# Performance work log

Measured on AMD Instinct MI355X. Metric: run time of the kernel, lower is better.

The kernel has to match this reference:

```python
import jax, jax.numpy as jnp
from jax import lax
import numpy as np
import math

B = 8
DIFF_LEN, HORIZON, NUM_NODES = 336, 96, 1024
SEG_LEN, D_CONV, D_MODEL = 8, 64, 128
NUM_KERNELS, DEPTH, ALPHA = 6, 2, 0.05
FREQ = math.ceil(DIFF_LEN / SEG_LEN)      # 42
STEP = math.ceil(HORIZON / SEG_LEN)       # 12
PAD = SEG_LEN * FREQ - DIFF_LEN           # 0 here, code stays general
MAXK = 2 * NUM_KERNELS - 1                # 11


def setup_inputs() -> dict:
    key = jax.random.key(0)
    ks = iter(jax.random.split(key, 64))
    p = lambda *s: 0.02 * jax.random.normal(next(ks), s, jnp.float32)
    inp = dict(
        x_diff=jax.random.normal(next(ks), (B, DIFF_LEN, NUM_NODES), jnp.float32),
        adj=jax.random.uniform(next(ks), (NUM_NODES, NUM_NODES), jnp.float32),
        enc_w1=p(SEG_LEN, D_MODEL), enc_b1=p(D_MODEL),
        enc_w2=p(D_MODEL, D_CONV), enc_b2=p(D_CONV),
        dec_w1=p(D_CONV, D_MODEL), dec_b1=p(D_MODEL),
        dec_w2=p(D_MODEL, SEG_LEN), dec_b2=p(SEG_LEN),
        g1_w=p((DEPTH + 1) * D_CONV, D_CONV), g1_b=p(D_CONV),
        g2_w=p((DEPTH + 1) * D_CONV, D_CONV), g2_b=p(D_CONV),
    )
    for i in range(NUM_KERNELS):
        inp[f'conv_w{i}'] = p(D_CONV, D_CONV, 1, 2 * i + 1)
        inp[f'conv_b{i}'] = p(D_CONV)
    return inp


def _mlp(x, w1, b1, w2, b2):
    # 2-hidden-layer MLP with ReLU (dropout = identity at eval)
    return jnp.maximum(x @ w1 + b1, 0.0) @ w2 + b2


def _t_inception(x, conv_ws, conv_bs):
    # x: (B, D, N, T); inception = mean of 'same'-padded (1, 2i+1) convs
    out = jnp.zeros_like(x)
    for i, (w, b) in enumerate(zip(conv_ws, conv_bs)):
        out = out + lax.conv_general_dilated(
            x, w, (1, 1), ((0, 0), (i, i)),
            dimension_numbers=('NCHW', 'OIHW', 'NCHW')) + b[None, :, None, None]
    return out / len(conv_ws)


def _norm_adj(adj):
    a = adj + jnp.eye(adj.shape[0], dtype=adj.dtype)
    return a / a.sum(1, keepdims=True)


def _mixprop(x, a, w, b):
    # x: (B, T, N, D), a: row-normalized (N, N)
    h = x
    outs = [h]
    for _ in range(DEPTH):
        h = ALPHA * x + (1.0 - ALPHA) * jnp.einsum('vn,btnd->btvd', a, h)
        outs.append(h)
    return jnp.concatenate(outs, -1) @ w + b


def _stconv(x, a1, a2, conv_ws, conv_bs, g1_w, g1_b, g2_w, g2_b):
    res = jnp.transpose(x, (0, 3, 2, 1))            # b d n t
    res = _t_inception(res, conv_ws, conv_bs)
    res = jnp.transpose(res, (0, 3, 2, 1))          # b t n d
    res = _mixprop(res, a1, g1_w, g1_b) + _mixprop(res, a2, g2_w, g2_b)
    return res + x                                   # dropout = identity at eval


def reference(x_diff, adj,
              enc_w1, enc_b1, enc_w2, enc_b2,
              dec_w1, dec_b1, dec_w2, dec_b2,
              g1_w, g1_b, g2_w, g2_b,
              conv_w0, conv_b0, conv_w1, conv_b1, conv_w2, conv_b2,
              conv_w3, conv_b3, conv_w4, conv_b4, conv_w5, conv_b5):
    conv_ws = [conv_w0, conv_w1, conv_w2, conv_w3, conv_w4, conv_w5]
    conv_bs = [conv_b0, conv_b1, conv_b2, conv_b3, conv_b4, conv_b5]
    Bb, L, N = x_diff.shape
    a1 = _norm_adj(adj)
    a2 = _norm_adj(adj.T)

    # segment + left-pad with tail so length = FREQ * SEG_LEN
    res = jnp.concatenate((x_diff[:, L - PAD:, :], x_diff), axis=1)
    res = res.reshape(Bb, FREQ, SEG_LEN, N)
    res = jnp.transpose(res, (0, 1, 3, 2))          # (B, F, N, P)
    res = _mlp(res, enc_w1, enc_b1, enc_w2, enc_b2)  # (B, F, N, D)

    # reconstruction branch (teacher-forced one-step shift)
    rec = jnp.concatenate(
        (res[:, :1],
         _stconv(res[:, :-1], a1, a2, conv_ws, conv_bs, g1_w, g1_b, g2_w, g2_b)),
        axis=1)
    rec = _mlp(rec, dec_w1, dec_b1, dec_w2, dec_b2)  # (B, F, N, P)
    rec = jnp.transpose(rec, (0, 1, 3, 2)).reshape(Bb, FREQ * SEG_LEN, N)
    rec = rec[:, -DIFF_LEN:, :]

    cur = res[:, -MAXK:]                             # (B, MAXK, N, D)
    preds = []
    for _ in range(STEP):
        p = _stconv(cur, a1, a2, conv_ws, conv_bs, g1_w, g1_b, g2_w, g2_b)[:, -1:]
        preds.append(p)
        cur = jnp.concatenate((cur[:, 1:], p), axis=1)
    pred = jnp.concatenate(preds, axis=1)            # (B, STEP, N, D)
    pred = _mlp(pred, dec_w1, dec_b1, dec_w2, dec_b2)  # (B, STEP, N, SEG)
    # NOTE: original torch code does a raw .reshape (not transpose); replicate it
    pred = pred.reshape(Bb, STEP * SEG_LEN, N)[:, :HORIZON, :]
    return (rec, pred)
```

## Files before the change

### kernel.cpp

```cpp
#include <hip/hip_runtime.h>

typedef __bf16 bf16;
typedef __bf16 bf16x8 __attribute__((ext_vector_type(8)));
typedef float f32x4 __attribute__((ext_vector_type(4)));

#define N_NODES 1024
#define DC 64
#define FREQ 42
#define TREC 41
#define NB 8
#define MAXK 11
#define NSTEP 12
#define SLICE 65536

__global__ void transpose_k(const float* __restrict__ in, float* __restrict__ out) {
  __shared__ float tile[32][33];
  int bx = blockIdx.x * 32, by = blockIdx.y * 32;
  int x = threadIdx.x, y = threadIdx.y;
#pragma unroll
  for (int j = 0; j < 32; j += 8) tile[y + j][x] = in[(size_t)(by + y + j) * N_NODES + bx + x];
  __syncthreads();
#pragma unroll
  for (int j = 0; j < 32; j += 8) out[(size_t)(bx + y + j) * N_NODES + by + x] = tile[x][y + j];
}

__global__ void rowsum_k(const float* __restrict__ m, float* __restrict__ sums) {
  int v = blockIdx.x;
  float s = 0.f;
  for (int n = threadIdx.x; n < N_NODES; n += 256) s += m[(size_t)v * N_NODES + n];
  __shared__ float red[256];
  red[threadIdx.x] = s;
  __syncthreads();
  for (int w = 128; w > 0; w >>= 1) {
    if (threadIdx.x < w) red[threadIdx.x] += red[threadIdx.x + w];
    __syncthreads();
  }
  if (threadIdx.x == 0) sums[v] = red[0] + 1.0f;
}

__global__ void norm_k(const float* __restrict__ adj, const float* __restrict__ adjT,
                       const float* __restrict__ rs, const float* __restrict__ cs,
                       bf16* __restrict__ a1, bf16* __restrict__ a2) {
  int v = blockIdx.x & (N_NODES - 1);
  bool second = blockIdx.x >= N_NODES;
  const float* src = second ? adjT : adj;
  float inv = 1.0f / (second ? cs[v] : rs[v]);
  bf16* dst = second ? a2 : a1;
  for (int n = threadIdx.x; n < N_NODES; n += 256) {
    float val = src[(size_t)v * N_NODES + n] + (n == v ? 1.0f : 0.0f);
    dst[(size_t)v * N_NODES + n] = (bf16)(val * inv);
  }
}

__global__ __launch_bounds__(256) void btrans_k(const bf16* __restrict__ src,
                                                bf16* __restrict__ dst) {
  __shared__ __align__(16) bf16 t[64][72];
  int bx = blockIdx.x * 64, by = blockIdx.y * 64;
  int tid = threadIdx.x;
#pragma unroll
  for (int i = 0; i < 2; ++i) {
    int q = tid + i * 256;
    int r = q >> 3, c = (q & 7) * 8;
    *(uint4*)&t[r][c] = *(const uint4*)&src[(size_t)(by + r) * N_NODES + bx + c];
  }
  __syncthreads();
#pragma unroll
  for (int i = 0; i < 2; ++i) {
    int q = tid + i * 256;
    int rr = q >> 3, cc = (q & 7) * 8;
    bf16 tmp[8];
#pragma unroll
    for (int e = 0; e < 8; ++e) tmp[e] = t[cc + e][rr];
    *(uint4*)&dst[(size_t)(bx + rr) * N_NODES + by + cc] = *(uint4*)tmp;
  }
}

__global__ void combine_w_k(const float* w0, const float* w1, const float* w2, const float* w3,
                            const float* w4, const float* w5, const float* b0, const float* b1,
                            const float* b2, const float* b3, const float* b4, const float* b5,
                            bf16* __restrict__ Wc, float* __restrict__ bsum) {
  int idx = blockIdx.x * 256 + threadIdx.x;
  if (idx < MAXK * 4096) {
    int dtI = idx >> 12;
    int dout = (idx >> 6) & 63;
    int di = idx & 63;
    int d = dtI - 5;
    int ad = d < 0 ? -d : d;
    const float* ws[6] = {w0, w1, w2, w3, w4, w5};
    float s = 0.f;
    for (int i = 0; i < 6; ++i)
      if (i >= ad) {
        int K = 2 * i + 1;
        s += ws[i][((size_t)dout * 64 + di) * K + (d + i)];
      }
    Wc[idx] = (bf16)s;
  }
  if (idx < 64) bsum[idx] = b0[idx] + b1[idx] + b2[idx] + b3[idx] + b4[idx] + b5[idx];
}

__global__ void vt_k(const float* __restrict__ g1w, const float* __restrict__ g2w,
                     const float* __restrict__ g1b, const float* __restrict__ g2b,
                     bf16* __restrict__ Vt, float* __restrict__ gbsum) {
  int idx = blockIdx.x * 256 + threadIdx.x;
  if (idx < 64) gbsum[idx] = g1b[idx] + g2b[idx];
  if (idx >= 5 * 4096) return;
  int j = idx >> 12;
  int dout = (idx >> 6) & 63;
  int din = idx & 63;
  const float al = 0.05f, bt = 0.95f;
  float v;
  if (j == 0)
    v = g1w[din * 64 + dout] + g2w[din * 64 + dout] +
        al * (g1w[(64 + din) * 64 + dout] + g1w[(128 + din) * 64 + dout] +
              g2w[(64 + din) * 64 + dout] + g2w[(128 + din) * 64 + dout]);
  else if (j == 1)
    v = bt * g1w[(64 + din) * 64 + dout] + al * bt * g1w[(128 + din) * 64 + dout];
  else if (j == 2)
    v = bt * bt * g1w[(128 + din) * 64 + dout];
  else if (j == 3)
    v = bt * g2w[(64 + din) * 64 + dout] + al * bt * g2w[(128 + din) * 64 + dout];
  else
    v = bt * bt * g2w[(128 + din) * 64 + dout];
  Vt[idx] = (bf16)v;
}

__global__ void prep_misc_k(const float* __restrict__ w2, const float* __restrict__ dw1,
                            const float* __restrict__ dw2, bf16* __restrict__ w2T,
                            bf16* __restrict__ dw1T, bf16* __restrict__ dw2T) {
  int i = blockIdx.x * 256 + threadIdx.x;
  if (i < 8192) {
    int dout = i >> 7, j = i & 127;
    w2T[i] = (bf16)w2[(size_t)j * 64 + dout];
    int jj = i >> 6, k = i & 63;
    dw1T[i] = (bf16)dw1[k * 128 + jj];
  }
  if (i < 2048) {
    int s = i >> 7, j = i & 127;
    dw2T[i] = (s < 8) ? (bf16)dw2[j * 8 + s] : (bf16)0.f;
  }
}

__global__ __launch_bounds__(256) void encoder_k(const float* __restrict__ x,
                                                 const float* __restrict__ w1,
                                                 const float* __restrict__ b1,
                                                 const bf16* __restrict__ w2T,
                                                 const float* __restrict__ b2,
                                                 bf16* __restrict__ resb,
                                                 float* __restrict__ cur,
                                                 bf16* __restrict__ curb) {
  __shared__ __align__(16) float xs[8 * 64];
  __shared__ __align__(16) float w1s[8 * 128];
  __shared__ float b1s[128];
  __shared__ float b2s[64];
  __shared__ __align__(16) bf16 hA[64 * 136];
  __shared__ __align__(16) bf16 wB[64 * 136];
  int tid = threadIdx.x;
  int v0 = blockIdx.x * 64;
  int bfp = blockIdx.y;
  int b = bfp / FREQ, f = bfp % FREQ;
#pragma unroll
  for (int i = 0; i < 2; ++i) {
    int q = tid + i * 256;
    xs[q] = x[(size_t)(b * 336 + f * 8 + (q >> 6)) * 1024 + v0 + (q & 63)];
  }
#pragma unroll
  for (int i = 0; i < 4; ++i) {
    int q = tid + i * 256;
    w1s[q] = w1[q];
  }
#pragma unroll
  for (int i = 0; i < 4; ++i) {
    int q = tid + i * 256;
    int dout = q >> 4, jc = (q & 15) * 8;
    *(uint4*)&wB[dout * 136 + jc] = *(const uint4*)&w2T[dout * 128 + jc];
  }
  if (tid < 128) b1s[tid] = b1[tid];
  if (tid < 64) b2s[tid] = b2[tid];
  __syncthreads();
  {
    int n = tid & 63, jc = (tid >> 6) * 32;
    for (int jj = 0; jj < 32; ++jj) {
      int j = jc + jj;
      float a = b1s[j];
#pragma unroll
      for (int k = 0; k < 8; ++k) a = fmaf(xs[k * 64 + n], w1s[k * 128 + j], a);
      hA[n * 136 + j] = (bf16)fmaxf(a, 0.f);
    }
  }
  __syncthreads();
  int wid = tid >> 6, lane = tid & 63, lr = lane & 15, lg = lane >> 4;
  f32x4 acc[4] = {};
#pragma unroll
  for (int ks = 0; ks < 4; ++ks) {
    bf16x8 a = *(const bf16x8*)&hA[(wid * 16 + lr) * 136 + ks * 32 + lg * 8];
#pragma unroll
    for (int ni = 0; ni < 4; ++ni) {
      bf16x8 bb = *(const bf16x8*)&wB[(ni * 16 + lr) * 136 + ks * 32 + lg * 8];
      acc[ni] = __builtin_amdgcn_mfma_f32_16x16x32_bf16(a, bb, acc[ni], 0, 0, 0);
    }
  }
  __syncthreads();
#pragma unroll
  for (int ni = 0; ni < 4; ++ni) {
    int n = ni * 16 + lr;
    float bz = b2s[n];
#pragma unroll
    for (int r = 0; r < 4; ++r) wB[(wid * 16 + lg * 4 + r) * 72 + n] = (bf16)(acc[ni][r] + bz);
  }
  __syncthreads();
  size_t so = (size_t)(b * FREQ + f) * SLICE;
#pragma unroll
  for (int i = 0; i < 2; ++i) {
    int q = tid + i * 256;
    int r = q >> 3, c = (q & 7) * 8;
    uint4 v = *(uint4*)&wB[r * 72 + c];
    *(uint4*)&resb[so + (size_t)(v0 + r) * 64 + c] = v;
    if (f >= 31) {
      size_t co = ((size_t)b * MAXK + (f - 31)) * SLICE + (size_t)(v0 + r) * 64 + c;
      *(uint4*)&curb[co] = v;
      bf16 tmp[8];
      *(uint4*)tmp = v;
      float4 fa, fb;
      fa.x = (float)tmp[0]; fa.y = (float)tmp[1]; fa.z = (float)tmp[2]; fa.w = (float)tmp[3];
      fb.x = (float)tmp[4]; fb.y = (float)tmp[5]; fb.z = (float)tmp[6]; fb.w = (float)tmp[7];
      *(float4*)&cur[co] = fa;
      *(float4*)&cur[co + 4] = fb;
    }
  }
}

__device__ __forceinline__ void stageA(bf16* lds_a, const bf16* src, int rowStride, int tid) {
#pragma unroll
  for (int i = 0; i < 8; ++i) {
    int q = tid + i * 256;
    int r = q >> 3, c = (q & 7) << 3;
    *(uint4*)&lds_a[r * 72 + c] = *(const uint4*)&src[(size_t)r * rowStride + c];
  }
}
__device__ __forceinline__ void stageB(bf16* lds_b, const bf16* src, int rowStride, int tid) {
#pragma unroll
  for (int i = 0; i < 2; ++i) {
    int q = tid + i * 256;
    int r = q >> 3, c = (q & 7) << 3;
    *(uint4*)&lds_b[r * 72 + c] = *(const uint4*)&src[(size_t)r * rowStride + c];
  }
}
__device__ __forceinline__ void mfma64(const bf16* lds_a, const bf16* lds_b, int wid, int lane,
                                       f32x4 acc[4][4]) {
  int lr = lane & 15, lg = lane >> 4;
#pragma unroll
  for (int h = 0; h < 2; ++h) {
    bf16x8 af[4], bfr[4];
#pragma unroll
    for (int mi = 0; mi < 4; ++mi)
      af[mi] = *(const bf16x8*)&lds_a[(wid * 64 + mi * 16 + lr) * 72 + h * 32 + lg * 8];
#pragma unroll
    for (int ni = 0; ni < 4; ++ni)
      bfr[ni] = *(const bf16x8*)&lds_b[(ni * 16 + lr) * 72 + h * 32 + lg * 8];
#pragma unroll
    for (int mi = 0; mi < 4; ++mi)
#pragma unroll
      for (int ni = 0; ni < 4; ++ni)
        acc[mi][ni] =
            __builtin_amdgcn_mfma_f32_16x16x32_bf16(af[mi], bfr[ni], acc[mi][ni], 0, 0, 0);
  }
}

__global__ __launch_bounds__(256) void asq_k(const bf16* __restrict__ a,
                                             const bf16* __restrict__ aT,
                                             bf16* __restrict__ out) {
  __shared__ __align__(16) bf16 As[64 * 72];
  __shared__ __align__(16) bf16 Bs2[64 * 72];
  int tid = threadIdx.x, w = tid >> 6, lane = tid & 63;
  int lr = lane & 15, lg = lane >> 4;
  int v0 = blockIdx.x * 64, n0 = blockIdx.y * 64;
  f32x4 acc[4] = {};
  for (int k0 = 0; k0 < 1024; k0 += 64) {
    __syncthreads();
    stageB(As, a + (size_t)v0 * 1024 + k0, 1024, tid);
    stageB(Bs2, aT + (size_t)n0 * 1024 + k0, 1024, tid);
    __syncthreads();
#pragma unroll
    for (int h = 0; h < 2; ++h) {
      bf16x8 av = *(const bf16x8*)&As[(w * 16 + lr) * 72 + h * 32 + lg * 8];
#pragma unroll
      for (int ni = 0; ni < 4; ++ni) {
        bf16x8 bv = *(const bf16x8*)&Bs2[(ni * 16 + lr) * 72 + h * 32 + lg * 8];
        acc[ni] = __builtin_amdgcn_mfma_f32_16x16x32_bf16(av, bv, acc[ni], 0, 0, 0);
      }
    }
  }
#pragma unroll
  for (int ni = 0; ni < 4; ++ni)
#pragma unroll
    for (int r = 0; r < 4; ++r) As[(w * 16 + lg * 4 + r) * 72 + ni * 16 + lr] = (bf16)acc[ni][r];
  __syncthreads();
#pragma unroll
  for (int i = 0; i < 2; ++i) {
    int q = tid + i * 256;
    int r = q >> 3, c = (q & 7) * 8;
    *(uint4*)&out[(size_t)(v0 + r) * 1024 + n0 + c] = *(uint4*)&As[r * 72 + c];
  }
}

__global__ __launch_bounds__(256) void incep_k(const bf16* __restrict__ resb, int b0,
                                               const bf16* __restrict__ Wc,
                                               const float* __restrict__ bsum,
                                               bf16* __restrict__ xcN, bf16* __restrict__ xcF) {
  __shared__ __align__(16) bf16 lds_a[256 * 72];
  __shared__ __align__(16) bf16 lds_b[64 * 72];
  int tid = threadIdx.x, wid = tid >> 6, lane = tid & 63;
  int v0 = blockIdx.x * 256;
  int sl = blockIdx.y;
  int b = b0 + sl / TREC, tt = sl % TREC;
  f32x4 acc[4][4] = {};
  for (int dt = 0; dt < MAXK; ++dt) {
    int ts = tt + dt - 5;
    if (ts < 0 || ts >= TREC) continue;
    __syncthreads();
    stageA(lds_a, resb + (size_t)(b * FREQ + ts) * SLICE + (size_t)v0 * 64, 64, tid);
    stageB(lds_b, Wc + dt * 4096, 64, tid);
    __syncthreads();
    mfma64(lds_a, lds_b, wid, lane, acc);
  }
  int lr = lane & 15, lg = lane >> 4;
  size_t so = (size_t)sl * SLICE;
  __syncthreads();
#pragma unroll
  for (int mi = 0; mi < 4; ++mi)
#pragma unroll
    for (int ni = 0; ni < 4; ++ni) {
      int n = ni * 16 + lr;
      float bs = bsum[n];
      union { bf16 h[4]; uint2 u; } pk;
#pragma unroll
      for (int r = 0; r < 4; ++r) {
        int m = wid * 64 + mi * 16 + lg * 4 + r;
        bf16 bv = (bf16)((acc[mi][ni][r] + bs) * (1.f / 6.f));
        lds_a[m * 72 + n] = bv;
        pk.h[r] = bv;
      }
      *(uint2*)&xcF[so + (size_t)n * 1024 + v0 + wid * 64 + mi * 16 + lg * 4] = pk.u;
    }
  __syncthreads();
#pragma unroll
  for (int i = 0; i < 8; ++i) {
    int q = tid + i * 256;
    int r = q >> 3, c = (q & 7) * 8;
    *(uint4*)&xcN[so + (size_t)(v0 + r) * 64 + c] = *(uint4*)&lds_a[r * 72 + c];
  }
}

__global__ __launch_bounds__(256) void fusedrec_k(
    const bf16* __restrict__ xcN, const bf16* __restrict__ xcF, const bf16* __restrict__ a1,
    const bf16* __restrict__ a1q, const bf16* __restrict__ a2, const bf16* __restrict__ a2q,
    const bf16* __restrict__ Vt, const float* __restrict__ gbsum,
    const bf16* __restrict__ resb, int b0, const bf16* __restrict__ dw1T,
    const float* __restrict__ db1, const bf16* __restrict__ dw2T,
    const float* __restrict__ db2, float* __restrict__ outRec) {
  __shared__ __align__(16) bf16 reg1[4][64 * 72];
  __shared__ __align__(16) bf16 reg2[64 * 72];
  __shared__ __align__(16) bf16 valb[64 * 72];
  bf16* hb = &reg1[0][0];
  int tid = threadIdx.x, w = tid >> 6, lane = tid & 63;
  int lr = lane & 15, lg = lane >> 4;
  int v0 = blockIdx.x * 64;
  int sy = blockIdx.y;
  int bl = sy / FREQ, f = sy % FREQ;
  int b = b0 + bl;

  if (f == 0) {
    const bf16* src = resb + (size_t)(b * FREQ) * SLICE + (size_t)v0 * 64;
#pragma unroll
    for (int i = 0; i < 2; ++i) {
      int q = tid + i * 256;
      int r = q >> 3, c = (q & 7) * 8;
      *(uint4*)&valb[r * 72 + c] = *(const uint4*)&src[(size_t)r * 64 + c];
    }
    __syncthreads();
  } else {
    int tt = f - 1;
    size_t so = (size_t)(bl * TREC + tt) * SLICE;
    f32x4 acc[4][4] = {};
    for (int k0 = 0; k0 < 1024; k0 += 64) {
      __syncthreads();
#pragma unroll
      for (int i = 0; i < 8; ++i) {
        int q = tid + i * 256;
        int mm = q >> 9, pos = q & 511;
        int rr = pos >> 3, cc = (pos & 7) * 8;
        const bf16* mp = mm == 0 ? a1 : (mm == 1 ? a1q : (mm == 2 ? a2 : a2q));
        *(uint4*)&reg1[mm][rr * 72 + cc] = *(const uint4*)&mp[(size_t)(v0 + rr) * 1024 + k0 + cc];
      }
#pragma unroll
      for (int i = 0; i < 2; ++i) {
        int q = tid + i * 256;
        int rb = q >> 3, cbb = (q & 7) * 8;
        *(uint4*)&reg2[rb * 72 + cbb] = *(const uint4*)&xcF[so + (size_t)rb * 1024 + k0 + cbb];
      }
      __syncthreads();
#pragma unroll
      for (int h = 0; h < 2; ++h) {
        bf16x8 af[4], bfr[4];
#pragma unroll
        for (int mi = 0; mi < 4; ++mi)
          af[mi] = *(const bf16x8*)&reg1[w][(mi * 16 + lr) * 72 + h * 32 + lg * 8];
#pragma unroll
        for (int ni = 0; ni < 4; ++ni)
          bfr[ni] = *(const bf16x8*)&reg2[(ni * 16 + lr) * 72 + h * 32 + lg * 8];
#pragma unroll
        for (int mi = 0; mi < 4; ++mi)
#pragma unroll
          for (int ni = 0; ni < 4; ++ni)
            acc[mi][ni] =
                __builtin_amdgcn_mfma_f32_16x16x32_bf16(af[mi], bfr[ni], acc[mi][ni], 0, 0, 0);
      }
    }
    __syncthreads();
#pragma unroll
    for (int mi = 0; mi < 4; ++mi)
#pragma unroll
      for (int ni = 0; ni < 4; ++ni)
#pragma unroll
        for (int r = 0; r < 4; ++r)
          reg1[w][(mi * 16 + lg * 4 + r) * 72 + ni * 16 + lr] = (bf16)acc[mi][ni][r];
#pragma unroll
    for (int i = 0; i < 2; ++i) {
      int q = tid + i * 256;
      int r = q >> 3, c = (q & 7) * 8;
      *(uint4*)&reg2[r * 72 + c] = *(const uint4*)&xcN[so + (size_t)(v0 + r) * 64 + c];
    }
    __syncthreads();
    f32x4 z[4] = {};
#pragma unroll
    for (int j = 0; j < 5; ++j) {
      const bf16* Asrc = (j == 0) ? reg2 : &reg1[j - 1][0];
#pragma unroll
      for (int h = 0; h < 2; ++h) {
        bf16x8 a = *(const bf16x8*)&Asrc[(w * 16 + lr) * 72 + h * 32 + lg * 8];
#pragma unroll
        for (int ni = 0; ni < 4; ++ni) {
          bf16x8 bb =
              *(const bf16x8*)&Vt[(size_t)j * 4096 + (ni * 16 + lr) * 64 + h * 32 + lg * 8];
          z[ni] = __builtin_amdgcn_mfma_f32_16x16x32_bf16(a, bb, z[ni], 0, 0, 0);
        }
      }
    }
    const bf16* xb = resb + (size_t)(b * FREQ + tt) * SLICE + (size_t)v0 * 64;
#pragma unroll
    for (int ni = 0; ni < 4; ++ni) {
      int n = ni * 16 + lr;
      float gb = gbsum[n];
#pragma unroll
      for (int r = 0; r < 4; ++r) {
        int m = w * 16 + lg * 4 + r;
        valb[m * 72 + n] = (bf16)((float)xb[(size_t)m * 64 + n] + z[ni][r] + gb);
      }
    }
    __syncthreads();
  }
  f32x4 hacc[4][2] = {};
#pragma unroll
  for (int h = 0; h < 2; ++h) {
    bf16x8 a[4];
#pragma unroll
    for (int mi = 0; mi < 4; ++mi)
      a[mi] = *(const bf16x8*)&valb[(mi * 16 + lr) * 72 + h * 32 + lg * 8];
#pragma unroll
    for (int ni2 = 0; ni2 < 2; ++ni2) {
      bf16x8 bb = *(const bf16x8*)&dw1T[(w * 32 + ni2 * 16 + lr) * 64 + h * 32 + lg * 8];
#pragma unroll
      for (int mi = 0; mi < 4; ++mi)
        hacc[mi][ni2] = __builtin_amdgcn_mfma_f32_16x16x32_bf16(a[mi], bb, hacc[mi][ni2], 0, 0, 0);
    }
  }
  __syncthreads();
#pragma unroll
  for (int ni2 = 0; ni2 < 2; ++ni2) {
    int j = w * 32 + ni2 * 16 + lr;
    float bz = db1[j];
#pragma unroll
    for (int mi = 0; mi < 4; ++mi)
#pragma unroll
      for (int r = 0; r < 4; ++r)
        hb[(mi * 16 + lg * 4 + r) * 136 + j] = (bf16)fmaxf(hacc[mi][ni2][r] + bz, 0.f);
  }
  __syncthreads();
  f32x4 oacc = {};
#pragma unroll
  for (int kc = 0; kc < 4; ++kc) {
    bf16x8 a = *(const bf16x8*)&hb[(w * 16 + lr) * 136 + kc * 32 + lg * 8];
    bf16x8 bb = *(const bf16x8*)&dw2T[lr * 128 + kc * 32 + lg * 8];
    oacc = __builtin_amdgcn_mfma_f32_16x16x32_bf16(a, bb, oacc, 0, 0, 0);
  }
  if (lr < 8) {
    float bz = db2[lr];
    float4 o;
    o.x = oacc[0] + bz;
    o.y = oacc[1] + bz;
    o.z = oacc[2] + bz;
    o.w = oacc[3] + bz;
    *(float4*)&outRec[(size_t)b * 344064 + (size_t)(f * 8 + lr) * 1024 + v0 + w * 16 + lg * 4] =
        o;
  }
}

__device__ __forceinline__ void arrive_wait(unsigned* c, int tid) {
  __syncthreads();
  if (tid == 0) {
    __hip_atomic_fetch_add(c, 1u, __ATOMIC_RELAXED, __HIP_MEMORY_SCOPE_AGENT);
    while (__hip_atomic_load(c, __ATOMIC_RELAXED, __HIP_MEMORY_SCOPE_AGENT) < 64u)
      __builtin_amdgcn_s_sleep(8);
  }
  __syncthreads();
}

__device__ __forceinline__ void incep16(const bf16* __restrict__ curb,
                                        const bf16* __restrict__ Wc, const float* bsums_,
                                        int base, int b, int r0, int w, int lr, int lg,
                                        bf16* yL, bf16* yFdst) {
  f32x4 ya = {};
  for (int j = 0; j < 6; ++j) {
    int slot = (base + 5 + j) % MAXK;
    const bf16* cb = curb + ((size_t)b * MAXK + slot) * SLICE + (size_t)r0 * 64;
#pragma unroll
    for (int h = 0; h < 2; ++h) {
      bf16x8 a = *(const bf16x8*)&cb[lr * 64 + h * 32 + lg * 8];
      bf16x8 bb = *(const bf16x8*)&Wc[(size_t)j * 4096 + (w * 16 + lr) * 64 + h * 32 + lg * 8];
      ya = __builtin_amdgcn_mfma_f32_16x16x32_bf16(a, bb, ya, 0, 0, 0);
    }
  }
  int n = w * 16 + lr;
  float bs = bsums_[n];
  union { bf16 h[4]; unsigned long long u; } pk;
#pragma unroll
  for (int r = 0; r < 4; ++r) {
    int m = lg * 4 + r;
    bf16 bv = (bf16)((ya[r] + bs) * (1.f / 6.f));
    yL[m * 72 + n] = bv;
    pk.h[r] = bv;
  }
  __hip_atomic_store((unsigned long long*)(yFdst + (size_t)n * 1024 + r0 + lg * 4), pk.u,
                     __ATOMIC_RELAXED, __HIP_MEMORY_SCOPE_AGENT);
}

struct AR5 {
  const bf16 *Wc;
  const float *bsum;
  const bf16 *a1, *a1q, *a2, *a2q;
  const bf16 *Vt;
  const float *gbsum;
  float *cur;
  bf16 *curb;
  bf16 *yF;
  const bf16 *dw1T;
  const float *db1;
  const bf16 *dw2T;
  const float *db2;
  float *outPred;
  unsigned *bar;
};

__global__ void __launch_bounds__(256) ar6_k(AR5 p) {
  __shared__ __align__(16) bf16 As4[2][4][16 * 72];
  __shared__ __align__(16) bf16 Bs[2][64 * 72];
  __shared__ __align__(16) bf16 yL[16 * 72];
  __shared__ __align__(16) bf16 PL[4][16 * 72];
  __shared__ __align__(16) bf16 valb[16 * 72];
  __shared__ __align__(16) bf16 hb[16 * 136];
  __shared__ float db1s[128], db2s[8], bsums[64], gbsums[64];
  int tid = threadIdx.x, w = tid >> 6, lane = tid & 63;
  int lr = lane & 15, lg = lane >> 4;
  int bid = blockIdx.x, b = bid >> 6, l = bid & 63;
  unsigned* cnt = p.bar + b * 32;
  int r0 = l * 16;

  if (tid < 128) db1s[tid] = p.db1[tid];
  if (tid < 8) db2s[tid] = p.db2[tid];
  if (tid < 64) {
    bsums[tid] = p.bsum[tid];
    gbsums[tid] = p.gbsum[tid];
  }
  __syncthreads();

  incep16(p.curb, p.Wc, bsums, 0, b, r0, w, lr, lg, yL, p.yF + (size_t)b * SLICE);
  arrive_wait(cnt + 0, tid);

  const bf16* mats[4] = {p.a1, p.a1q, p.a2, p.a2q};
  for (int s = 0; s < NSTEP; ++s) {
    {
      const bf16* yFs = p.yF + ((size_t)s * NB + b) * SLICE;
      f32x4 acc[4] = {};
      auto stage_chunk = [&](int d, int k0) {
#pragma unroll
        for (int i = 0; i < 2; ++i) {
          int q = tid + i * 256;
          int mm = q >> 7, rr = (q >> 3) & 15, cc = (q & 7) * 8;
          *(uint4*)&As4[d][mm][rr * 72 + cc] =
              *(const uint4*)&mats[mm][(size_t)(r0 + rr) * 1024 + k0 + cc];
          int rb = q >> 3, cb2 = (q & 7) * 8;
          *(uint4*)&Bs[d][rb * 72 + cb2] = *(const uint4*)&yFs[(size_t)rb * 1024 + k0 + cb2];
        }
      };
      stage_chunk(0, 0);
      for (int c = 0; c < 16; ++c) {
        __syncthreads();
        if (c < 15) stage_chunk((c + 1) & 1, (c + 1) * 64);
#pragma unroll
        for (int h = 0; h < 2; ++h) {
          bf16x8 a = *(const bf16x8*)&As4[c & 1][w][lr * 72 + h * 32 + lg * 8];
#pragma unroll
          for (int ni = 0; ni < 4; ++ni) {
            bf16x8 bb = *(const bf16x8*)&Bs[c & 1][(ni * 16 + lr) * 72 + h * 32 + lg * 8];
            acc[ni] = __builtin_amdgcn_mfma_f32_16x16x32_bf16(a, bb, acc[ni], 0, 0, 0);
          }
        }
      }
#pragma unroll
      for (int ni = 0; ni < 4; ++ni) {
        int nn = ni * 16 + lr;
#pragma unroll
        for (int r = 0; r < 4; ++r) PL[w][(lg * 4 + r) * 72 + nn] = (bf16)acc[ni][r];
      }
    }
    __syncthreads();
    {
      f32x4 z = {};
#pragma unroll
      for (int j = 0; j < 5; ++j) {
        const bf16* Aj = (j == 0) ? yL : PL[j - 1];
#pragma unroll
        for (int h = 0; h < 2; ++h) {
          bf16x8 a = *(const bf16x8*)&Aj[lr * 72 + h * 32 + lg * 8];
          bf16x8 bb =
              *(const bf16x8*)&p.Vt[(size_t)j * 4096 + (w * 16 + lr) * 64 + h * 32 + lg * 8];
          z = __builtin_amdgcn_mfma_f32_16x16x32_bf16(a, bb, z, 0, 0, 0);
        }
      }
      int slotR = (s + 10) % MAXK, slotW = s % MAXK;
      size_t xo = ((size_t)b * MAXK + slotR) * SLICE + (size_t)r0 * 64;
      size_t wo = ((size_t)b * MAXK + slotW) * SLICE + (size_t)r0 * 64;
      int n = w * 16 + lr;
      float gb = gbsums[n];
#pragma unroll
      for (int r = 0; r < 4; ++r) {
        int m = lg * 4 + r;
        size_t o = (size_t)m * 64 + n;
        float v = p.cur[xo + o] + z[r] + gb;
        p.cur[wo + o] = v;
        p.curb[wo + o] = (bf16)v;
        valb[m * 72 + n] = (bf16)v;
      }
      __syncthreads();
      if (s < NSTEP - 1)
        incep16(p.curb, p.Wc, bsums, s + 1, b, r0, w, lr, lg, yL,
                p.yF + ((size_t)(s + 1) * NB + b) * SLICE);
      f32x4 hacc[2] = {};
#pragma unroll
      for (int h = 0; h < 2; ++h) {
        bf16x8 a = *(const bf16x8*)&valb[lr * 72 + h * 32 + lg * 8];
#pragma unroll
        for (int ni2 = 0; ni2 < 2; ++ni2) {
          bf16x8 bb = *(const bf16x8*)&p.dw1T[(w * 32 + ni2 * 16 + lr) * 64 + h * 32 + lg * 8];
          hacc[ni2] = __builtin_amdgcn_mfma_f32_16x16x32_bf16(a, bb, hacc[ni2], 0, 0, 0);
        }
      }
#pragma unroll
      for (int ni2 = 0; ni2 < 2; ++ni2) {
        int j = w * 32 + ni2 * 16 + lr;
        float bz = db1s[j];
#pragma unroll
        for (int r = 0; r < 4; ++r)
          hb[(lg * 4 + r) * 136 + j] = (bf16)fmaxf(hacc[ni2][r] + bz, 0.f);
      }
      __syncthreads();
      f32x4 oacc = {};
#pragma unroll
      for (int kc = 0; kc < 4; ++kc) {
        bf16x8 a = *(const bf16x8*)&hb[lr * 136 + kc * 32 + lg * 8];
        bf16x8 bb = *(const bf16x8*)&p.dw2T[lr * 128 + kc * 32 + lg * 8];
        oacc = __builtin_amdgcn_mfma_f32_16x16x32_bf16(a, bb, oacc, 0, 0, 0);
      }
      if (w == 0 && lr < 8) {
        float bz = db2s[lr];
#pragma unroll
        for (int r = 0; r < 4; ++r)
          p.outPred[(size_t)b * 98304 + (size_t)s * 8192 + (size_t)(r0 + lg * 4 + r) * 8 + lr] =
              oacc[r] + bz;
      }
    }
    if (s < NSTEP - 1) arrive_wait(cnt + 1 + s, tid);
  }
}

extern "C" void kernel_launch(void* const* d_in, const int* in_sizes, int n_in, void* d_out,
                              int out_size, void* d_ws, size_t ws_size, hipStream_t stream) {
  const float* x_diff = (const float*)d_in[0];
  const float* adj = (const float*)d_in[1];
  const float* enc_w1 = (const float*)d_in[2];
  const float* enc_b1 = (const float*)d_in[3];
  const float* enc_w2 = (const float*)d_in[4];
  const float* enc_b2 = (const float*)d_in[5];
  const float* dec_w1 = (const float*)d_in[6];
  const float* dec_b1 = (const float*)d_in[7];
  const float* dec_w2 = (const float*)d_in[8];
  const float* dec_b2 = (const float*)d_in[9];
  const float* g1_w = (const float*)d_in[10];
  const float* g1_b = (const float*)d_in[11];
  const float* g2_w = (const float*)d_in[12];
  const float* g2_b = (const float*)d_in[13];
  const float* cw[6];
  const float* cb_[6];
  for (int i = 0; i < 6; ++i) {
    cw[i] = (const float*)d_in[14 + 2 * i];
    cb_[i] = (const float*)d_in[15 + 2 * i];
  }

  char* base = (char*)d_ws;
  size_t off = 0;
  auto alloc = [&](size_t bytes) -> void* {
    void* p = base + off;
    off = (off + bytes + 255) & ~(size_t)255;
    return p;
  };
  float* adjT = (float*)alloc(1048576ULL * 4);
  float* rowsum = (float*)alloc(4096);
  float* colsum = (float*)alloc(4096);
  bf16* a1b = (bf16*)alloc(1048576ULL * 2);
  bf16* a2b = (bf16*)alloc(1048576ULL * 2);
  bf16* a1T = (bf16*)alloc(1048576ULL * 2);
  bf16* a2T = (bf16*)alloc(1048576ULL * 2);
  bf16* a1q = (bf16*)alloc(1048576ULL * 2);
  bf16* a2q = (bf16*)alloc(1048576ULL * 2);
  bf16* Wc = (bf16*)alloc(45056ULL * 2);
  float* bsum = (float*)alloc(256);
  float* gbsum = (float*)alloc(256);
  bf16* Vt = (bf16*)alloc(20480ULL * 2);
  bf16* w2T = (bf16*)alloc(8192ULL * 2);
  bf16* dw1T = (bf16*)alloc(8192ULL * 2);
  bf16* dw2T = (bf16*)alloc(2048ULL * 2);
  bf16* resb = (bf16*)alloc((size_t)NB * FREQ * SLICE * 2);
  float* cur = (float*)alloc((size_t)NB * MAXK * SLICE * 4);
  bf16* curb = (bf16*)alloc((size_t)NB * MAXK * SLICE * 2);
  bf16* yF = (bf16*)alloc((size_t)NSTEP * NB * SLICE * 2);
  unsigned* gbar = (unsigned*)alloc(4096);
  size_t fixedEnd = off;
  int cb = NB;
  while (cb > 1) {
    size_t S = (size_t)TREC * cb;
    if (fixedEnd + S * SLICE * 4 + 65536 <= ws_size) break;
    cb >>= 1;
  }
  size_t S = (size_t)TREC * cb;
  bf16* xcN = (bf16*)alloc(S * SLICE * 2);
  bf16* xcF = (bf16*)alloc(S * SLICE * 2);

  float* outF = (float*)d_out;
  float* outRec = outF;
  float* outPred = outF + (size_t)2752512;

  transpose_k<<<dim3(32, 32), dim3(32, 8), 0, stream>>>(adj, adjT);
  rowsum_k<<<1024, 256, 0, stream>>>(adj, rowsum);
  rowsum_k<<<1024, 256, 0, stream>>>(adjT, colsum);
  norm_k<<<2048, 256, 0, stream>>>(adj, adjT, rowsum, colsum, a1b, a2b);
  btrans_k<<<dim3(16, 16), 256, 0, stream>>>(a1b, a1T);
  btrans_k<<<dim3(16, 16), 256, 0, stream>>>(a2b, a2T);
  asq_k<<<dim3(16, 16), 256, 0, stream>>>(a1b, a1T, a1q);
  asq_k<<<dim3(16, 16), 256, 0, stream>>>(a2b, a2T, a2q);
  combine_w_k<<<(MAXK * 4096 + 255) / 256, 256, 0, stream>>>(cw[0], cw[1], cw[2], cw[3], cw[4],
                                                             cw[5], cb_[0], cb_[1], cb_[2],
                                                             cb_[3], cb_[4], cb_[5], Wc, bsum);
  vt_k<<<80, 256, 0, stream>>>(g1_w, g2_w, g1_b, g2_b, Vt, gbsum);
  prep_misc_k<<<32, 256, 0, stream>>>(enc_w2, dec_w1, dec_w2, w2T, dw1T, dw2T);
  encoder_k<<<dim3(16, NB * FREQ), 256, 0, stream>>>(x_diff, enc_w1, enc_b1, w2T, enc_b2,
                                                     resb, cur, curb);

  for (int c0 = 0; c0 < NB; c0 += cb) {
    int Sg = TREC * cb;
    incep_k<<<dim3(4, Sg), 256, 0, stream>>>(resb, c0, Wc, bsum, xcN, xcF);
    fusedrec_k<<<dim3(16, cb * FREQ), 256, 0, stream>>>(xcN, xcF, a1b, a1q, a2b, a2q, Vt,
                                                        gbsum, resb, c0, dw1T, dec_b1, dw2T,
                                                        dec_b2, outRec);
  }

  hipMemsetAsync(gbar, 0, 4096, stream);
  AR5 arp;
  arp.Wc = Wc; arp.bsum = bsum;
  arp.a1 = a1b; arp.a1q = a1q; arp.a2 = a2b; arp.a2q = a2q;
  arp.Vt = Vt; arp.gbsum = gbsum;
  arp.cur = cur; arp.curb = curb;
  arp.yF = yF;
  arp.dw1T = dw1T; arp.db1 = dec_b1; arp.dw2T = dw2T; arp.db2 = dec_b2;
  arp.outPred = outPred;
  arp.bar = gbar;
  ar6_k<<<dim3(512), dim3(256), 0, stream>>>(arp);
}
```

Before: 816.5 us.

## Prefetch adjacency tiles into registers and double-buffer xcF tiles in fusedrec

In the fused reconstruction kernel, each wave now owns one of the four adjacency matrices. It prefetches the next 64x64 k-tile of that matrix into registers while MFMAs run on the current tile. The xcF operand tile is double-buffered in LDS, which cuts the per-iteration barriers from two to one. This aims to hide global-load latency in the main mixprop GEMM loop, at the cost of about 32 extra VGPRs per thread and one more LDS buffer, which may lower occupancy.

Result: slower. 1.317 ms (+61.3%).

```diff
diff --git a/kernel.cpp b/kernel.cpp
--- a/kernel.cpp
+++ b/kernel.cpp
@@ -359,7 +359,7 @@
     const float* __restrict__ db1, const bf16* __restrict__ dw2T,
     const float* __restrict__ db2, float* __restrict__ outRec) {
   __shared__ __align__(16) bf16 reg1[4][64 * 72];
-  __shared__ __align__(16) bf16 reg2[64 * 72];
+  __shared__ __align__(16) bf16 reg2[2][64 * 72];
   __shared__ __align__(16) bf16 valb[64 * 72];
   bf16* hb = &reg1[0][0];
   int tid = threadIdx.x, w = tid >> 6, lane = tid & 63;
@@ -381,24 +381,42 @@
   } else {
     int tt = f - 1;
     size_t so = (size_t)(bl * TREC + tt) * SLICE;
+    const bf16* mp = w == 0 ? a1 : (w == 1 ? a1q : (w == 2 ? a2 : a2q));
+    const bf16* mprow = mp + (size_t)v0 * 1024;
+    int pr = lane >> 3, pc = (lane & 7) * 8;
+    uint4 pref[8];
+#pragma unroll
+    for (int i = 0; i < 8; ++i)
+      pref[i] = *(const uint4*)&mprow[(size_t)(i * 8 + pr) * 1024 + pc];
+#pragma unroll
+    for (int i = 0; i < 2; ++i) {
+      int q = tid + i * 256;
+      int rb = q >> 3, cbb = (q & 7) * 8;
+      *(uint4*)&reg2[0][rb * 72 + cbb] = *(const uint4*)&xcF[so + (size_t)rb * 1024 + cbb];
+    }
     f32x4 acc[4][4] = {};
-    for (int k0 = 0; k0 < 1024; k0 += 64) {
+    for (int c = 0; c < 16; ++c) {
       __syncthreads();
-#pragma unroll
-      for (int i = 0; i < 8; ++i) {
-        int q = tid + i * 256;
-        int mm = q >> 9, pos = q & 511;
-        int rr = pos >> 3, cc = (pos & 7) * 8;
-        const bf16* mp = mm == 0 ? a1 : (mm == 1 ? a1q : (mm == 2 ? a2 : a2q));
-        *(uint4*)&reg1[mm][rr * 72 + cc] = *(const uint4*)&mp[(size_t)(v0 + rr) * 1024 + k0 + cc];
-      }
-#pragma unroll
-      for (int i = 0; i < 2; ++i) {
-        int q = tid + i * 256;
-        int rb = q >> 3, cbb = (q & 7) * 8;
-        *(uint4*)&reg2[rb * 72 + cbb] = *(const uint4*)&xcF[so + (size_t)rb * 1024 + k0 + cbb];
-      }
-      __syncthreads();
+      if (c < 15) {
+        int k0n = (c + 1) * 64;
+#pragma unroll
+        for (int i = 0; i < 2; ++i) {
+          int q = tid + i * 256;
+          int rb = q >> 3, cbb = (q & 7) * 8;
+          *(uint4*)&reg2[(c + 1) & 1][rb * 72 + cbb] =
+              *(const uint4*)&xcF[so + (size_t)rb * 1024 + k0n + cbb];
+        }
+      }
+#pragma unroll
+      for (int i = 0; i < 8; ++i)
+        *(uint4*)&reg1[w][(i * 8 + pr) * 72 + pc] = pref[i];
+      if (c < 15) {
+        int k0n = (c + 1) * 64;
+#pragma unroll
+        for (int i = 0; i < 8; ++i)
+          pref[i] = *(const uint4*)&mprow[(size_t)(i * 8 + pr) * 1024 + k0n + pc];
+      }
+      const bf16* b2 = &reg2[c & 1][0];
 #pragma unroll
       for (int h = 0; h < 2; ++h) {
         bf16x8 af[4], bfr[4];
@@ -407,7 +425,7 @@
           af[mi] = *(const bf16x8*)&reg1[w][(mi * 16 + lr) * 72 + h * 32 + lg * 8];
 #pragma unroll
         for (int ni = 0; ni < 4; ++ni)
-          bfr[ni] = *(const bf16x8*)&reg2[(ni * 16 + lr) * 72 + h * 32 + lg * 8];
+          bfr[ni] = *(const bf16x8*)&b2[(ni * 16 + lr) * 72 + h * 32 + lg * 8];
 #pragma unroll
         for (int mi = 0; mi < 4; ++mi)
 #pragma unroll
@@ -428,13 +446,13 @@
     for (int i = 0; i < 2; ++i) {
       int q = tid + i * 256;
       int r = q >> 3, c = (q & 7) * 8;
-      *(uint4*)&reg2[r * 72 + c] = *(const uint4*)&xcN[so + (size_t)(v0 + r) * 64 + c];
+      *(uint4*)&reg2[0][r * 72 + c] = *(const uint4*)&xcN[so + (size_t)(v0 + r) * 64 + c];
     }
     __syncthreads();
     f32x4 z[4] = {};
 #pragma unroll
     for (int j = 0; j < 5; ++j) {
-      const bf16* Asrc = (j == 0) ? reg2 : &reg1[j - 1][0];
+      const bf16* Asrc = (j == 0) ? &reg2[0][0] : &reg1[j - 1][0];
 #pragma unroll
       for (int h = 0; h < 2; ++h) {
         bf16x8 a = *(const bf16x8*)&Asrc[(w * 16 + lr) * 72 + h * 32 + lg * 8];
```
